# Optimization experiments

Measured on AMD Instinct MI355X. Metric: run time of the kernel, lower is better.

Reference implementation:

```python
import jax, jax.numpy as jnp
import numpy as np

WS = (2, 7, 7)          # window size (s, h, w)
DIM = 192
HEADS = 6
HEAD_DIM = DIM // HEADS
N = WS[0] * WS[1] * WS[2]  # 98
TABLE = (2 * WS[0] - 1) * (2 * WS[1] - 1) * (2 * WS[2] - 1)  # 507


def _relative_position_index():
    coords = np.stack(np.meshgrid(np.arange(WS[0]), np.arange(WS[1]), np.arange(WS[2]), indexing='ij'))
    cf = coords.reshape(3, -1)                      # [3, N]
    rel = cf[:, :, None] - cf[:, None, :]           # [3, N, N]
    rel = rel.transpose(1, 2, 0).astype(np.int64)   # [N, N, 3]
    rel[..., 0] += WS[0] - 1
    rel[..., 1] += WS[1] - 1
    rel[..., 2] += WS[2] - 1
    rel[..., 0] *= 3 * WS[1] - 1  # faithful to source (quirky multiplier)
    rel[..., 1] *= 2 * WS[1] - 1
    return jnp.asarray(rel.sum(-1), dtype=jnp.int32)  # [N, N]


def setup_inputs() -> dict:
    key = jax.random.key(0)
    ks = jax.random.split(key, 8)
    B_ = 1024
    nW = 64
    skip = jax.random.normal(ks[0], (B_, N, DIM), dtype=jnp.float32)
    x_up = jax.random.normal(ks[1], (B_, N, DIM), dtype=jnp.float32)
    mask = jax.random.normal(ks[2], (nW, N, N), dtype=jnp.float32)
    kv_w = jax.random.normal(ks[3], (DIM, 2 * DIM), dtype=jnp.float32) * 0.02
    kv_b = jnp.zeros((2 * DIM,), dtype=jnp.float32)
    proj_w = jax.random.normal(ks[4], (DIM, DIM), dtype=jnp.float32) * 0.02
    proj_b = jnp.zeros((DIM,), dtype=jnp.float32)
    rpb_table = jax.random.normal(ks[5], (TABLE, HEADS), dtype=jnp.float32) * 0.02
    rel_idx = _relative_position_index()
    return {"skip": skip, "x_up": x_up, "mask": mask, "kv_w": kv_w, "kv_b": kv_b,
            "proj_w": proj_w, "proj_b": proj_b, "rpb_table": rpb_table, "rel_idx": rel_idx}


def reference(skip, x_up, mask, kv_w, kv_b, proj_w, proj_b, rpb_table, rel_idx):
    B_, n, C = skip.shape
    nW = mask.shape[0]
    scale = HEAD_DIM ** -0.5
    kv = skip @ kv_w + kv_b                                # [B_, N, 2C]
    kv = kv.reshape(B_, n, 2, HEADS, HEAD_DIM)
    k = kv[:, :, 0]                                        # [B_, N, H, hd]
    v = kv[:, :, 1]
    q = x_up.reshape(B_, n, HEADS, HEAD_DIM) * scale
    attn = jnp.einsum('bqhd,bkhd->bhqk', q, k)             # [B_, H, N, N]
    bias = rpb_table[rel_idx]                              # [N, N, H]
    attn = attn + jnp.transpose(bias, (2, 0, 1))[None]
    attn = attn.reshape(B_ // nW, nW, HEADS, n, n) + mask[None, :, None]
    attn = attn.reshape(B_, HEADS, n, n)
    attn = jax.nn.softmax(attn, axis=-1)
    out = jnp.einsum('bhqk,bkhd->bqhd', attn, v).reshape(B_, n, C)
    return out @ proj_w + proj_b
```

## Files before the change

### kernel.cpp

```cpp
#include <hip/hip_runtime.h>

#define NTOK 98
#define DIM 192
#define HEADS 6
#define SCALE 0.17677669529663687f

using shortx8 = __attribute__((ext_vector_type(8))) short;
using floatx4 = __attribute__((ext_vector_type(4))) float;

static __device__ __forceinline__ unsigned short f2bf(float f) {
    unsigned u = __float_as_uint(f);
    u += 0x7FFFu + ((u >> 16) & 1u);
    return (unsigned short)(u >> 16);
}

static __device__ __forceinline__ shortx8 pack8(const float* p, float scale) {
    float4 a = *(const float4*)p;
    float4 b = *(const float4*)(p + 4);
    shortx8 t;
    t[0] = (short)f2bf(a.x * scale); t[1] = (short)f2bf(a.y * scale);
    t[2] = (short)f2bf(a.z * scale); t[3] = (short)f2bf(a.w * scale);
    t[4] = (short)f2bf(b.x * scale); t[5] = (short)f2bf(b.y * scale);
    t[6] = (short)f2bf(b.z * scale); t[7] = (short)f2bf(b.w * scale);
    return t;
}

__global__ void prep_kernel(const float* __restrict__ rpb, const int* __restrict__ relidx,
                            const float* __restrict__ kvw, const float* __restrict__ pw,
                            float* __restrict__ biasF, unsigned short* __restrict__ kvB,
                            unsigned short* __restrict__ pB) {
    int e = blockIdx.x * 256 + threadIdx.x;
    if (e < HEADS * NTOK * NTOK) {
        int h = e / (NTOK * NTOK), ij = e % (NTOK * NTOK);
        biasF[e] = rpb[relidx[ij] * HEADS + h];
    }
    if (e < 73728) {
        int jj = e & 7, lane = (e >> 3) & 63, t = e >> 9;
        int NT = t % 24, ks = t / 24;
        int c = ks * 32 + (lane >> 4) * 8 + jj;
        int n = NT * 16 + (lane & 15);
        kvB[e] = f2bf(kvw[c * 384 + n]);
    }
    if (e < 36864) {
        int jj = e & 7, lane = (e >> 3) & 63, t = e >> 9;
        int NT = t % 12, ks = t / 12;
        int c = ks * 32 + (lane >> 4) * 8 + jj;
        int n = NT * 16 + (lane & 15);
        pB[e] = f2bf(pw[c * 192 + n]);
    }
}

__global__ __launch_bounds__(448, 2) void fused_kernel(
    const float* __restrict__ skip, const float* __restrict__ xup,
    const float* __restrict__ mask, const float* __restrict__ kv_b,
    const float* __restrict__ biasF, const unsigned short* __restrict__ kvB,
    const unsigned short* __restrict__ pB, const float* __restrict__ pb,
    float* __restrict__ out) {

    __shared__ __align__(16) unsigned short lds[37376];
    unsigned short* kB3 = lds;
    unsigned short* vB3 = lds + 10752;
    unsigned short* PAb = lds + 23040;

    const int tid  = threadIdx.x;
    const int w    = tid >> 6;
    const int lane = tid & 63;
    const int l15  = lane & 15;
    const int quad = lane >> 4;
    const int win  = blockIdx.x;

    for (int e = tid; e < 6 * 512; e += 448)
        vB3[(e >> 9) * 2048 + 3 * 512 + (e & 511)] = 0;
    for (int e = tid; e < 7 * 256; e += 448)
        PAb[(e >> 8) * 2048 + 3 * 512 + 256 + (e & 255)] = 0;
    __syncthreads();

    const int mA  = w * 16 + l15;
    const int mAc = mA < NTOK ? mA : 97;

    const float* mw = mask + (size_t)(win & 63) * NTOK * NTOK;
    unsigned opk[12][2];

    #pragma unroll
    for (int g = 0; g < 2; ++g) {
        if (g) __syncthreads();

        {
            shortx8 afr[6];
            const float* sr = skip + ((size_t)win * NTOK + mAc) * DIM + quad * 8;
            #pragma unroll
            for (int ks = 0; ks < 6; ++ks) afr[ks] = pack8(sr + ks * 32, 1.0f);
            #pragma unroll
            for (int nt = 0; nt < 12; ++nt) {
                const int NTg = (nt < 6) ? (6 * g + nt) : (6 + 6 * g + nt);
                const float cb = kv_b[NTg * 16 + l15];
                floatx4 acc = {cb, cb, cb, cb};
                #pragma unroll
                for (int ks = 0; ks < 6; ++ks) {
                    shortx8 bf = *(const shortx8*)(kvB + ((size_t)((ks * 24 + NTg) * 64 + lane)) * 8);
                    acc = __builtin_amdgcn_mfma_f32_16x16x32_bf16(afr[ks], bf, acc, 0, 0, 0);
                }
                if (nt < 6) {
                    const int ch = nt * 16 + l15, hh = ch >> 5, dh = ch & 31;
                    const int base = ((hh * 7 + w) * 64) * 8 + (dh & 7);
                    const int lphi = ((dh >> 3) & 3) << 4;
                    #pragma unroll
                    for (int r = 0; r < 4; ++r) {
                        int mm = quad * 4 + r;
                        kB3[base + (mm | lphi) * 8] = f2bf(acc[r]);
                    }
                } else {
                    const int cv = (nt - 6) * 16 + l15, hh = cv >> 5, dh = cv & 31, ntv = dh >> 4;
                    #pragma unroll
                    for (int r = 0; r < 4; ++r) {
                        int m = w * 16 + quad * 4 + r;
                        if (m < NTOK) {
                            int lp = (dh & 15) | (((m >> 3) & 3) << 4);
                            vB3[(((hh * 2 + ntv) * 4 + (m >> 5)) * 64 + lp) * 8 + (m & 7)] = f2bf(acc[r]);
                        }
                    }
                }
            }
        }
        __syncthreads();

        #pragma unroll
        for (int hp = 0; hp < 3; ++hp) {
            const int h = 3 * g + hp;
            shortx8 qf = pack8(xup + ((size_t)win * NTOK + mAc) * DIM + h * 32 + quad * 8, SCALE);

            floatx4 S[7];
            const float* bh = biasF + h * NTOK * NTOK;
            #pragma unroll
            for (int nt = 0; nt < 7; ++nt) {
                const int j = nt * 16 + l15;
                #pragma unroll
                for (int r = 0; r < 4; ++r) {
                    int i = w * 16 + quad * 4 + r;
                    int ic = i < NTOK ? i : 97;
                    S[nt][r] = (j < NTOK) ? (bh[ic * NTOK + j] + mw[ic * NTOK + j]) : -1e30f;
                }
            }
            #pragma unroll
            for (int nt = 0; nt < 7; ++nt) {
                shortx8 bk = *(const shortx8*)&kB3[((hp * 7 + nt) * 64 + lane) * 8];
                S[nt] = __builtin_amdgcn_mfma_f32_16x16x32_bf16(qf, bk, S[nt], 0, 0, 0);
            }
            float inv[4];
            #pragma unroll
            for (int r = 0; r < 4; ++r) {
                float mx = S[0][r];
                #pragma unroll
                for (int nt = 1; nt < 7; ++nt) mx = fmaxf(mx, S[nt][r]);
                mx = fmaxf(mx, __shfl_xor(mx, 1));
                mx = fmaxf(mx, __shfl_xor(mx, 2));
                mx = fmaxf(mx, __shfl_xor(mx, 4));
                mx = fmaxf(mx, __shfl_xor(mx, 8));
                float sm = 0.f;
                #pragma unroll
                for (int nt = 0; nt < 7; ++nt) { float ev = __expf(S[nt][r] - mx); S[nt][r] = ev; sm += ev; }
                sm += __shfl_xor(sm, 1);
                sm += __shfl_xor(sm, 2);
                sm += __shfl_xor(sm, 4);
                sm += __shfl_xor(sm, 8);
                inv[r] = 1.0f / sm;
            }
            #pragma unroll
            for (int nt = 0; nt < 7; ++nt) {
                const int j = nt * 16 + l15;
                const int ks = nt >> 1;
                const int lphi = ((j >> 3) & 3) << 4;
                #pragma unroll
                for (int r = 0; r < 4; ++r) {
                    int mm = quad * 4 + r;
                    PAb[((w * 4 + ks) * 64 + (mm | lphi)) * 8 + (j & 7)] = f2bf(S[nt][r]);
                }
            }
            shortx8 pa[4];
            #pragma unroll
            for (int ks = 0; ks < 4; ++ks)
                pa[ks] = *(const shortx8*)&PAb[((w * 4 + ks) * 64 + lane) * 8];
            #pragma unroll
            for (int nt = 0; nt < 2; ++nt) {
                floatx4 o = {0.f, 0.f, 0.f, 0.f};
                #pragma unroll
                for (int ks = 0; ks < 4; ++ks) {
                    shortx8 vb = *(const shortx8*)&vB3[(((hp * 2 + nt) * 4 + ks) * 64 + lane) * 8];
                    o = __builtin_amdgcn_mfma_f32_16x16x32_bf16(pa[ks], vb, o, 0, 0, 0);
                }
                opk[h * 2 + nt][0] = (unsigned)f2bf(o[0] * inv[0]) | ((unsigned)f2bf(o[1] * inv[1]) << 16);
                opk[h * 2 + nt][1] = (unsigned)f2bf(o[2] * inv[2]) | ((unsigned)f2bf(o[3] * inv[3]) << 16);
            }
        }
    }

    __syncthreads();

    #pragma unroll
    for (int h = 0; h < 6; ++h)
        #pragma unroll
        for (int nt = 0; nt < 2; ++nt)
            #pragma unroll
            for (int r = 0; r < 4; ++r) {
                int mm = quad * 4 + r;
                int dsub = nt * 16 + l15;
                unsigned v = opk[h * 2 + nt][r >> 1] >> ((r & 1) * 16);
                lds[((w * 6 + h) * 64 + (mm | (((dsub >> 3) & 3) << 4))) * 8 + (dsub & 7)] =
                    (unsigned short)v;
            }

    shortx8 oa[6];
    #pragma unroll
    for (int ks = 0; ks < 6; ++ks)
        oa[ks] = *(const shortx8*)&lds[((w * 6 + ks) * 64 + lane) * 8];
    float* obase = out + (size_t)win * NTOK * DIM;
    #pragma unroll
    for (int nt = 0; nt < 12; ++nt) {
        const int n = nt * 16 + l15;
        const float bb = pb[n];
        floatx4 acc = {bb, bb, bb, bb};
        #pragma unroll
        for (int ks = 0; ks < 6; ++ks) {
            shortx8 bf = *(const shortx8*)(pB + ((size_t)((ks * 12 + nt) * 64 + lane)) * 8);
            acc = __builtin_amdgcn_mfma_f32_16x16x32_bf16(oa[ks], bf, acc, 0, 0, 0);
        }
        #pragma unroll
        for (int r = 0; r < 4; ++r) {
            int m = w * 16 + quad * 4 + r;
            if (m < NTOK) obase[m * DIM + n] = acc[r];
        }
    }
}

extern "C" void kernel_launch(void* const* d_in, const int* in_sizes, int n_in,
                              void* d_out, int out_size, void* d_ws, size_t ws_size,
                              hipStream_t stream) {
    const float* skip   = (const float*)d_in[0];
    const float* x_up   = (const float*)d_in[1];
    const float* mask   = (const float*)d_in[2];
    const float* kv_w   = (const float*)d_in[3];
    const float* kv_b   = (const float*)d_in[4];
    const float* proj_w = (const float*)d_in[5];
    const float* proj_b = (const float*)d_in[6];
    const float* rpb    = (const float*)d_in[7];
    const int*   relidx = (const int*)d_in[8];
    float* out = (float*)d_out;

    float*          biasF = (float*)d_ws;
    unsigned short* kvB   = (unsigned short*)((char*)d_ws + 230496);
    unsigned short* pB    = (unsigned short*)((char*)d_ws + 377952);

    prep_kernel<<<288, 256, 0, stream>>>(rpb, relidx, kv_w, proj_w, biasF, kvB, pB);
    fused_kernel<<<1024, 448, 0, stream>>>(skip, x_up, mask, kv_b, biasF, kvB, pB, proj_b, out);
}
```

Baseline: 404.6 us.

## Transpose attention tiles to keep P and O in registers via ds_bpermute

```diff
diff --git a/kernel.cpp b/kernel.cpp
--- a/kernel.cpp
+++ b/kernel.cpp
@@ -25,14 +25,47 @@
     return t;
 }
 
+static __device__ __forceinline__ shortx8 frag_from_words(unsigned w0, unsigned w1,
+                                                          unsigned w2, unsigned w3) {
+    union { unsigned u[4]; shortx8 s; } t;
+    t.u[0] = w0; t.u[1] = w1; t.u[2] = w2; t.u[3] = w3;
+    return t.s;
+}
+
+template <bool HI>
+static __device__ __forceinline__ shortx8 xchg4(unsigned lo0, unsigned lo1,
+                                                unsigned hi0, unsigned hi1,
+                                                int A0b, int A1b, bool hiSel) {
+    unsigned l0 = (unsigned)__builtin_amdgcn_ds_bpermute(A0b, (int)lo0);
+    unsigned l1 = (unsigned)__builtin_amdgcn_ds_bpermute(A0b, (int)lo1);
+    unsigned l2 = (unsigned)__builtin_amdgcn_ds_bpermute(A1b, (int)lo0);
+    unsigned l3 = (unsigned)__builtin_amdgcn_ds_bpermute(A1b, (int)lo1);
+    unsigned h0 = 0, h1 = 0, h2 = 0, h3 = 0;
+    if (HI) {
+        h0 = (unsigned)__builtin_amdgcn_ds_bpermute(A0b, (int)hi0);
+        h1 = (unsigned)__builtin_amdgcn_ds_bpermute(A0b, (int)hi1);
+        h2 = (unsigned)__builtin_amdgcn_ds_bpermute(A1b, (int)hi0);
+        h3 = (unsigned)__builtin_amdgcn_ds_bpermute(A1b, (int)hi1);
+    }
+    return frag_from_words(hiSel ? h0 : l0, hiSel ? h1 : l1,
+                           hiSel ? h2 : l2, hiSel ? h3 : l3);
+}
+
 __global__ void prep_kernel(const float* __restrict__ rpb, const int* __restrict__ relidx,
+                            const float* __restrict__ mask,
                             const float* __restrict__ kvw, const float* __restrict__ pw,
-                            float* __restrict__ biasF, unsigned short* __restrict__ kvB,
-                            unsigned short* __restrict__ pB) {
+                            float* __restrict__ biasT, float* __restrict__ maskT,
+                            unsigned short* __restrict__ kvB, unsigned short* __restrict__ pB) {
     int e = blockIdx.x * 256 + threadIdx.x;
     if (e < HEADS * NTOK * NTOK) {
-        int h = e / (NTOK * NTOK), ij = e % (NTOK * NTOK);
-        biasF[e] = rpb[relidx[ij] * HEADS + h];
+        int h = e / (NTOK * NTOK), rem = e % (NTOK * NTOK);
+        int j = rem / NTOK, i = rem % NTOK;
+        biasT[e] = rpb[relidx[i * NTOK + j] * HEADS + h];
+    }
+    if (e < 64 * NTOK * NTOK) {
+        int wd = e / (NTOK * NTOK), rem = e % (NTOK * NTOK);
+        int j = rem / NTOK, i = rem % NTOK;
+        maskT[e] = mask[((size_t)wd * NTOK + i) * NTOK + j];
     }
     if (e < 73728) {
         int jj = e & 7, lane = (e >> 3) & 63, t = e >> 9;
@@ -50,17 +83,16 @@
     }
 }
 
-__global__ __launch_bounds__(448, 2) void fused_kernel(
+__global__ __launch_bounds__(448, 3) void fused_kernel(
     const float* __restrict__ skip, const float* __restrict__ xup,
-    const float* __restrict__ mask, const float* __restrict__ kv_b,
-    const float* __restrict__ biasF, const unsigned short* __restrict__ kvB,
+    const float* __restrict__ kv_b,
+    const float* __restrict__ biasT, const float* __restrict__ maskT,
+    const unsigned short* __restrict__ kvB,
     const unsigned short* __restrict__ pB, const float* __restrict__ pb,
     float* __restrict__ out) {
 
-    __shared__ __align__(16) unsigned short lds[37376];
-    unsigned short* kB3 = lds;
-    unsigned short* vB3 = lds + 10752;
-    unsigned short* PAb = lds + 23040;
+    __shared__ __align__(16) unsigned short kB3[3 * 7 * 512];
+    __shared__ __align__(16) unsigned short vB3[3 * 2 * 4 * 512];
 
     const int tid  = threadIdx.x;
     const int w    = tid >> 6;
@@ -70,15 +102,15 @@
     const int win  = blockIdx.x;
 
     for (int e = tid; e < 6 * 512; e += 448)
-        vB3[(e >> 9) * 2048 + 3 * 512 + (e & 511)] = 0;
-    for (int e = tid; e < 7 * 256; e += 448)
-        PAb[(e >> 8) * 2048 + 3 * 512 + 256 + (e & 255)] = 0;
+        vB3[(e / 512) * 2048 + 3 * 512 + (e & 511)] = 0;
     __syncthreads();
 
     const int mA  = w * 16 + l15;
     const int mAc = mA < NTOK ? mA : 97;
 
-    const float* mw = mask + (size_t)(win & 63) * NTOK * NTOK;
+    const int A0b = ((32 * (quad & 1) + l15) << 2);
+    const int A1b = A0b + 64;
+
     unsigned opk[12][2];
 
     #pragma unroll
@@ -130,89 +162,82 @@
             shortx8 qf = pack8(xup + ((size_t)win * NTOK + mAc) * DIM + h * 32 + quad * 8, SCALE);
 
             floatx4 S[7];
-            const float* bh = biasF + h * NTOK * NTOK;
-            #pragma unroll
-            for (int nt = 0; nt < 7; ++nt) {
-                const int j = nt * 16 + l15;
+            {
+                const float* bT = biasT + (size_t)h * (NTOK * NTOK);
+                const float* mT = maskT + (size_t)(win & 63) * (NTOK * NTOK);
                 #pragma unroll
-                for (int r = 0; r < 4; ++r) {
-                    int i = w * 16 + quad * 4 + r;
-                    int ic = i < NTOK ? i : 97;
-                    S[nt][r] = (j < NTOK) ? (bh[ic * NTOK + j] + mw[ic * NTOK + j]) : -1e30f;
+                for (int nt = 0; nt < 7; ++nt) {
+                    #pragma unroll
+                    for (int r = 0; r < 4; ++r) {
+                        int j = nt * 16 + quad * 4 + r;
+                        S[nt][r] = (j < NTOK) ? (bT[j * NTOK + mAc] + mT[j * NTOK + mAc])
+                                              : -1e30f;
+                    }
                 }
             }
             #pragma unroll
             for (int nt = 0; nt < 7; ++nt) {
                 shortx8 bk = *(const shortx8*)&kB3[((hp * 7 + nt) * 64 + lane) * 8];
-                S[nt] = __builtin_amdgcn_mfma_f32_16x16x32_bf16(qf, bk, S[nt], 0, 0, 0);
-            }
-            float inv[4];
-            #pragma unroll
-            for (int r = 0; r < 4; ++r) {
-                float mx = S[0][r];
+                S[nt] = __builtin_amdgcn_mfma_f32_16x16x32_bf16(bk, qf, S[nt], 0, 0, 0);
+            }
+            float mx;
+            {
+                float m0 = fmaxf(fmaxf(S[0][0], S[0][1]), fmaxf(S[0][2], S[0][3]));
+                float m1 = fmaxf(fmaxf(S[1][0], S[1][1]), fmaxf(S[1][2], S[1][3]));
+                float m2 = fmaxf(fmaxf(S[2][0], S[2][1]), fmaxf(S[2][2], S[2][3]));
+                float m3 = fmaxf(fmaxf(S[3][0], S[3][1]), fmaxf(S[3][2], S[3][3]));
+                float m4 = fmaxf(fmaxf(S[4][0], S[4][1]), fmaxf(S[4][2], S[4][3]));
+                float m5 = fmaxf(fmaxf(S[5][0], S[5][1]), fmaxf(S[5][2], S[5][3]));
+                float m6 = fmaxf(fmaxf(S[6][0], S[6][1]), fmaxf(S[6][2], S[6][3]));
+                mx = fmaxf(fmaxf(fmaxf(m0, m1), fmaxf(m2, m3)), fmaxf(fmaxf(m4, m5), m6));
+                mx = fmaxf(mx, __shfl_xor(mx, 16));
+                mx = fmaxf(mx, __shfl_xor(mx, 32));
+            }
+            float sm = 0.f;
+            #pragma unroll
+            for (int nt = 0; nt < 7; ++nt) {
                 #pragma unroll
-                for (int nt = 1; nt < 7; ++nt) mx = fmaxf(mx, S[nt][r]);
-                mx = fmaxf(mx, __shfl_xor(mx, 1));
-                mx = fmaxf(mx, __shfl_xor(mx, 2));
-                mx = fmaxf(mx, __shfl_xor(mx, 4));
-                mx = fmaxf(mx, __shfl_xor(mx, 8));
-                float sm = 0.f;
-                #pragma unroll
-                for (int nt = 0; nt < 7; ++nt) { float ev = __expf(S[nt][r] - mx); S[nt][r] = ev; sm += ev; }
-                sm += __shfl_xor(sm, 1);
-                sm += __shfl_xor(sm, 2);
-                sm += __shfl_xor(sm, 4);
-                sm += __shfl_xor(sm, 8);
-                inv[r] = 1.0f / sm;
-            }
+                for (int r = 0; r < 4; ++r) { S[nt][r] = __expf(S[nt][r] - mx); }
+                sm += (S[nt][0] + S[nt][1]) + (S[nt][2] + S[nt][3]);
+            }
+            sm += __shfl_xor(sm, 16);
+            sm += __shfl_xor(sm, 32);
+            const float inv = 1.0f / sm;
+
+            unsigned pk[7][2];
             #pragma unroll
             for (int nt = 0; nt < 7; ++nt) {
-                const int j = nt * 16 + l15;
-                const int ks = nt >> 1;
-                const int lphi = ((j >> 3) & 3) << 4;
-                #pragma unroll
-                for (int r = 0; r < 4; ++r) {
-                    int mm = quad * 4 + r;
-                    PAb[((w * 4 + ks) * 64 + (mm | lphi)) * 8 + (j & 7)] = f2bf(S[nt][r]);
-                }
-            }
-            shortx8 pa[4];
-            #pragma unroll
-            for (int ks = 0; ks < 4; ++ks)
-                pa[ks] = *(const shortx8*)&PAb[((w * 4 + ks) * 64 + lane) * 8];
-            #pragma unroll
-            for (int nt = 0; nt < 2; ++nt) {
-                floatx4 o = {0.f, 0.f, 0.f, 0.f};
-                #pragma unroll
-                for (int ks = 0; ks < 4; ++ks) {
-                    shortx8 vb = *(const shortx8*)&vB3[(((hp * 2 + nt) * 4 + ks) * 64 + lane) * 8];
-                    o = __builtin_amdgcn_mfma_f32_16x16x32_bf16(pa[ks], vb, o, 0, 0, 0);
-                }
-                opk[h * 2 + nt][0] = (unsigned)f2bf(o[0] * inv[0]) | ((unsigned)f2bf(o[1] * inv[1]) << 16);
-                opk[h * 2 + nt][1] = (unsigned)f2bf(o[2] * inv[2]) | ((unsigned)f2bf(o[3] * inv[3]) << 16);
-            }
-        }
-    }
-
-    __syncthreads();
-
-    #pragma unroll
-    for (int h = 0; h < 6; ++h)
-        #pragma unroll
-        for (int nt = 0; nt < 2; ++nt)
-            #pragma unroll
-            for (int r = 0; r < 4; ++r) {
-                int mm = quad * 4 + r;
-                int dsub = nt * 16 + l15;
-                unsigned v = opk[h * 2 + nt][r >> 1] >> ((r & 1) * 16);
-                lds[((w * 6 + h) * 64 + (mm | (((dsub >> 3) & 3) << 4))) * 8 + (dsub & 7)] =
-                    (unsigned short)v;
-            }
-
+                pk[nt][0] = (unsigned)f2bf(S[nt][0]) | ((unsigned)f2bf(S[nt][1]) << 16);
+                pk[nt][1] = (unsigned)f2bf(S[nt][2]) | ((unsigned)f2bf(S[nt][3]) << 16);
+            }
+            floatx4 o0 = {0.f, 0.f, 0.f, 0.f}, o1 = {0.f, 0.f, 0.f, 0.f};
+            const bool hiSel = (quad & 2) != 0;
+            #pragma unroll
+            for (int ks = 0; ks < 4; ++ks) {
+                shortx8 pfr;
+                if (ks < 3)
+                    pfr = xchg4<true>(pk[2 * ks][0], pk[2 * ks][1],
+                                      pk[2 * ks + 1][0], pk[2 * ks + 1][1], A0b, A1b, hiSel);
+                else
+                    pfr = xchg4<false>(pk[6][0], pk[6][1], 0u, 0u, A0b, A1b, hiSel);
+                shortx8 vb0 = *(const shortx8*)&vB3[(((hp * 2 + 0) * 4 + ks) * 64 + lane) * 8];
+                o0 = __builtin_amdgcn_mfma_f32_16x16x32_bf16(vb0, pfr, o0, 0, 0, 0);
+                shortx8 vb1 = *(const shortx8*)&vB3[(((hp * 2 + 1) * 4 + ks) * 64 + lane) * 8];
+                o1 = __builtin_amdgcn_mfma_f32_16x16x32_bf16(vb1, pfr, o1, 0, 0, 0);
+            }
+            opk[h * 2 + 0][0] = (unsigned)f2bf(o0[0] * inv) | ((unsigned)f2bf(o0[1] * inv) << 16);
+            opk[h * 2 + 0][1] = (unsigned)f2bf(o0[2] * inv) | ((unsigned)f2bf(o0[3] * inv) << 16);
+            opk[h * 2 + 1][0] = (unsigned)f2bf(o1[0] * inv) | ((unsigned)f2bf(o1[1] * inv) << 16);
+            opk[h * 2 + 1][1] = (unsigned)f2bf(o1[2] * inv) | ((unsigned)f2bf(o1[3] * inv) << 16);
+        }
+    }
+
+    const bool hiSel = (quad & 2) != 0;
     shortx8 oa[6];
     #pragma unroll
-    for (int ks = 0; ks < 6; ++ks)
-        oa[ks] = *(const shortx8*)&lds[((w * 6 + ks) * 64 + lane) * 8];
+    for (int hh = 0; hh < 6; ++hh)
+        oa[hh] = xchg4<true>(opk[hh * 2][0], opk[hh * 2][1],
+                             opk[hh * 2 + 1][0], opk[hh * 2 + 1][1], A0b, A1b, hiSel);
     float* obase = out + (size_t)win * NTOK * DIM;
     #pragma unroll
     for (int nt = 0; nt < 12; ++nt) {
@@ -246,10 +271,13 @@
     const int*   relidx = (const int*)d_in[8];
     float* out = (float*)d_out;
 
-    float*          biasF = (float*)d_ws;
-    unsigned short* kvB   = (unsigned short*)((char*)d_ws + 230496);
-    unsigned short* pB    = (unsigned short*)((char*)d_ws + 377952);
-
-    prep_kernel<<<288, 256, 0, stream>>>(rpb, relidx, kv_w, proj_w, biasF, kvB, pB);
-    fused_kernel<<<1024, 448, 0, stream>>>(skip, x_up, mask, kv_b, biasF, kvB, pB, proj_b, out);
-}
+    float*          biasT = (float*)d_ws;
+    float*          maskT = (float*)((char*)d_ws + 230496);
+    unsigned short* kvB   = (unsigned short*)((char*)d_ws + 2689120);
+    unsigned short* pB    = (unsigned short*)((char*)d_ws + 2836576);
+
+    prep_kernel<<<2402, 256, 0, stream>>>(rpb, relidx, mask, kv_w, proj_w,
+                                          biasT, maskT, kvB, pB);
+    fused_kernel<<<1024, 448, 0, stream>>>(skip, x_up, kv_b, biasT, maskT, kvB, pB,
+                                           proj_b, out);
+}
```

Result: slower. 459.8 us (+13.7%).
